# Optimization experiments

Measured on AMD Instinct MI355X. Metric: run time of the kernel, lower is better.

The kernel has to match this reference:

```python
import jax, jax.numpy as jnp
import numpy as np

N, E, DIN, D, FE, L, B, M = 10000, 40000, 11, 64, 4, 4, 512, 3


def setup_inputs() -> dict:
    key = jax.random.key(0)
    ks = iter(jax.random.split(key, 24))
    s = lambda *sh: jax.random.normal(next(ks), sh, jnp.float32)
    return {
        "x": s(N, DIN),
        "edge_index": jax.random.randint(next(ks), (2, E), 0, N),
        "edge_attr": jax.random.uniform(next(ks), (E, FE), jnp.float32),
        "batch": jnp.sort(jax.random.randint(next(ks), (N,), 0, B)),
        "W0": s(DIN, D) * 0.1, "b0": jnp.zeros((D,), jnp.float32),
        "Wn1": s(FE, 2 * D) * 0.1, "bn1": jnp.zeros((2 * D,), jnp.float32),
        "Wn2": s(2 * D, D * D) * 0.02, "bn2": jnp.zeros((D * D,), jnp.float32),
        "root": s(L, D, D) * 0.1, "conv_bias": jnp.zeros((L, D), jnp.float32),
        "lstm_Wih": s(4 * D, 2 * D) * 0.1, "lstm_Whh": s(4 * D, D) * 0.1,
        "lstm_b": jnp.zeros((4 * D,), jnp.float32),
        "Wo1": s(2 * D, D) * 0.1, "bo1": jnp.zeros((D,), jnp.float32),
        "Wo2": s(D, 1) * 0.1, "bo2": jnp.zeros((1,), jnp.float32),
    }


def reference(x, edge_index, edge_attr, batch, W0, b0, Wn1, bn1, Wn2, bn2,
              root, conv_bias, lstm_Wih, lstm_Whh, lstm_b, Wo1, bo1, Wo2, bo2):
    src, dst = edge_index[0], edge_index[1]
    h = x @ W0 + b0  # [N, D]
    # Edge MLP is SHARED across all conv layers -> compute per-edge weight matrices once
    ew = (jax.nn.silu(edge_attr @ Wn1 + bn1) @ Wn2 + bn2).reshape(E, D, D)
    for l in range(L):
        msg = jnp.einsum('ed,edf->ef', h[src], ew)  # gather-compute per edge
        aggr = jax.ops.segment_sum(msg, dst, num_segments=N)  # scatter-add to targets
        h = h + (aggr + h @ root[l] + conv_bias[l])  # NNConv + residual
    # Set2Set pooling (LSTM, M processing steps)
    q_star = jnp.zeros((B, 2 * D), h.dtype)
    hs = jnp.zeros((B, D), h.dtype)
    cs = jnp.zeros((B, D), h.dtype)
    for _ in range(M):
        gates = q_star @ lstm_Wih.T + hs @ lstm_Whh.T + lstm_b
        i, f, g, o = jnp.split(gates, 4, axis=-1)  # torch LSTM gate order
        cs = jax.nn.sigmoid(f) * cs + jax.nn.sigmoid(i) * jnp.tanh(g)
        hs = jax.nn.sigmoid(o) * jnp.tanh(cs)
        q = hs  # [B, D]
        e = jnp.sum(h * q[batch], axis=-1)  # [N]
        emax = jax.ops.segment_max(e, batch, num_segments=B)
        ex = jnp.exp(e - emax[batch])
        denom = jax.ops.segment_sum(ex, batch, num_segments=B)
        a = ex / denom[batch]  # per-graph softmax attention
        r = jax.ops.segment_sum(a[:, None] * h, batch, num_segments=B)
        q_star = jnp.concatenate([q, r], axis=-1)
    out = jax.nn.silu(q_star @ Wo1 + bo1) @ Wo2 + bo2
    return out.reshape(-1)
```

## Files before the change

### kernel.cpp

```cpp
#include <hip/hip_runtime.h>
#include <cstdint>
#include <cstddef>

#define NN   10000
#define EE   40000
#define DIN_ 11
#define DD   64
#define LL   4
#define BB   512
#define MM   3
#define K1   128
#define DD2  4096
#define NPB  16
#define CSPL 2
#define CPB  4
#define ESLOT 12
#define ECREG (8 * ESLOT)
#define EHW (ECREG * 8)

typedef unsigned short ushort_t;
typedef unsigned int   uint_t;

typedef __bf16 bf16x8_t __attribute__((ext_vector_type(8)));
typedef float  f32x4_t  __attribute__((ext_vector_type(4)));
union FragU { uint4 u; bf16x8_t b; };

__device__ __forceinline__ float bfu(ushort_t u) { return __uint_as_float(((uint_t)u) << 16); }
__device__ __forceinline__ float bflo(uint_t u) { return __uint_as_float(u << 16); }
__device__ __forceinline__ float bfhi(uint_t u) { return __uint_as_float(u & 0xffff0000u); }
__device__ __forceinline__ ushort_t f2bf(float f) {
  uint_t u = __float_as_uint(f);
  u = (u + 0x7fffu + ((u >> 16) & 1u)) >> 16;
  return (ushort_t)u;
}
__device__ __forceinline__ uint_t pack2(float lo, float hi) {
  return (uint_t)f2bf(lo) | ((uint_t)f2bf(hi) << 16);
}
__device__ __forceinline__ float sigmf_(float x) { return 1.f / (1.f + expf(-x)); }
__device__ __forceinline__ float siluf_(float x) { return x / (1.f + expf(-x)); }

#if defined(__HIP_DEVICE_COMPILE__) && __has_builtin(__builtin_amdgcn_fdot2_f32_bf16)
typedef __bf16 bf16x2_t __attribute__((ext_vector_type(2)));
__device__ __forceinline__ float dot2a(uint_t a, uint_t b, float c) {
  union { uint_t u; bf16x2_t v; } ua, ub;
  ua.u = a; ub.u = b;
  return __builtin_amdgcn_fdot2_f32_bf16(ua.v, ub.v, c, false);
}
#else
__device__ __forceinline__ float dot2a(uint_t a, uint_t b, float c) {
  return c + bflo(a) * bflo(b) + bfhi(a) * bfhi(b);
}
#endif

#define NCANON 16
struct CanonArgs {
  const void* src[NCANON];
  float* dst[NCANON];
  int n[NCANON];
};
__global__ void k_canon(CanonArgs a, const ushort_t* __restrict__ ea, int* __restrict__ flag) {
  __shared__ int bad;
  if (threadIdx.x == 0) bad = 0;
  __syncthreads();
  ushort_t u = ea[threadIdx.x];
  if ((u & 0x8000u) || u > 0x3F80u) atomicAdd(&bad, 1);
  __syncthreads();
  const int isbf = (bad == 0) ? 1 : 0;
  if (blockIdx.x == 0 && blockIdx.y == 0 && threadIdx.x == 0) *flag = isbf;
  const int ai = blockIdx.y;
  const int n = a.n[ai];
  const int i = blockIdx.x * 256 + threadIdx.x;
  if (i >= n) return;
  float v;
  if (isbf) v = bfu(((const ushort_t*)a.src[ai])[i]);
  else      v = ((const float*)a.src[ai])[i];
  a.dst[ai][i] = v;
}

__global__ void k_wn2m(const void* __restrict__ Wn2, uint_t* __restrict__ out,
                       const int* __restrict__ flag) {
  __shared__ ushort_t row[DD2];
  const int k = blockIdx.x, tid = threadIdx.x;
  if (*flag) {
    const uint4* src = (const uint4*)((const ushort_t*)Wn2 + (size_t)k * DD2);
    ((uint4*)row)[tid] = src[tid];
    ((uint4*)row)[tid + 256] = src[tid + 256];
  } else {
    const float* src = (const float*)Wn2 + (size_t)k * DD2;
    for (int j = 0; j < 16; ++j) row[tid + 256 * j] = f2bf(src[tid + 256 * j]);
  }
  __syncthreads();
  const int kpg = k >> 1, par = k & 1;
  const int lane = tid >> 2, jp = tid & 3;
  const int q = lane >> 4, n = lane & 15;
  for (int fc = 0; fc < 4; ++fc) {
#pragma unroll
    for (int hf = 0; hf < 2; ++hf) {
      int d0 = hf * 32 + q * 8 + 2 * jp;
      int f = fc * 16 + n;
      uint_t lo = row[d0 * 64 + f], hi = row[(d0 + 1) * 64 + f];
      out[((((size_t)kpg * 4 + fc) * 2 + par) * 2 + hf) * 256 + tid] = lo | (hi << 16);
    }
  }
}

__global__ void k_wT(const float* __restrict__ Wihc, const float* __restrict__ Whhc,
                     float* __restrict__ Wiht, float* __restrict__ Whht) {
  int idx = blockIdx.x * 256 + threadIdx.x;
  if (idx < 4 * DD * K1) {
    int j = idx >> 7, i = idx & 127;
    Wiht[i * 256 + j] = Wihc[idx];
  }
  if (idx < 4 * DD * DD) {
    int j = idx >> 6, i = idx & 63;
    Whht[i * 256 + j] = Whhc[idx];
  }
}

__global__ __launch_bounds__(256) void k_embed(
    const float* __restrict__ x, const float* __restrict__ W0,
    const float* __restrict__ b0, const float* __restrict__ bn2,
    float* __restrict__ h, uint_t* __restrict__ hpk,
    float* __restrict__ nbias) {
  __shared__ float xs[4][DIN_];
  __shared__ float hl[4][DD];
  const int tid = threadIdx.x, w = tid >> 6, f = tid & 63;
  const int n = blockIdx.x * 4 + w;
  if (f < DIN_) xs[w][f] = x[n * DIN_ + f];
  __syncthreads();
  float a = b0[f];
  for (int i = 0; i < DIN_; ++i) a += xs[w][i] * W0[i * DD + f];
  h[(size_t)n * DD + f] = a;
  hl[w][f] = a;
  float other = __shfl_down(a, 1);
  if ((f & 1) == 0)
    hpk[(size_t)n * 32 + (f >> 1)] = pack2(a, other);
  __syncthreads();
  float nb = 0.f;
#pragma unroll
  for (int d = 0; d < DD; ++d) nb += hl[w][d] * bn2[d * DD + f];
  nbias[(size_t)n * DD + f] = nb;
}

__global__ void k_edgemlp(const float* __restrict__ ea, const float* __restrict__ Wn1,
                          const float* __restrict__ bn1, const int* __restrict__ epos,
                          uint_t* __restrict__ hn1c) {
  int idx = blockIdx.x * 256 + threadIdx.x;
  if (idx >= EE * (K1 / 2)) return;
  int e = idx >> 6, j = idx & 63;
  int k0 = 2 * j, k1 = 2 * j + 1;
  float a0 = ea[e * 4 + 0], a1 = ea[e * 4 + 1], a2 = ea[e * 4 + 2], a3 = ea[e * 4 + 3];
  float t0 = bn1[k0] + a0 * Wn1[k0] + a1 * Wn1[K1 + k0] + a2 * Wn1[2 * K1 + k0] + a3 * Wn1[3 * K1 + k0];
  float t1 = bn1[k1] + a0 * Wn1[k1] + a1 * Wn1[K1 + k1] + a2 * Wn1[2 * K1 + k1] + a3 * Wn1[3 * K1 + k1];
  int pos = epos[e];
  hn1c[((size_t)(j >> 3) * EE + pos) * 8 + (j & 7)] = pack2(siluf_(t0), siluf_(t1));
}

__global__ void k_hist(const int* __restrict__ ei, int* __restrict__ cnt_s) {
  int e = blockIdx.x * 256 + threadIdx.x;
  if (e >= EE) return;
  atomicAdd(&cnt_s[ei[e]], 1);
}

__global__ void k_scan(const int* __restrict__ cnt, int* __restrict__ rp,
                       const int* __restrict__ batch, int* __restrict__ goff) {
  if (blockIdx.x == 1) {
    int g = threadIdx.x;
    if (g > BB) return;
    int lo = 0, hi = NN;
    while (lo < hi) {
      int mid = (lo + hi) >> 1;
      if (batch[mid] < g) lo = mid + 1; else hi = mid;
    }
    goff[g] = lo;
    return;
  }
  __shared__ int part[1024];
  const int tid = threadIdx.x;
  const int chunk = (NN + 1023) / 1024;
  int s = 0;
  for (int j = 0; j < chunk; ++j) {
    int idx = tid * chunk + j;
    if (idx < NN) s += cnt[idx];
  }
  part[tid] = s;
  __syncthreads();
  for (int off = 1; off < 1024; off <<= 1) {
    int v = (tid >= off) ? part[tid - off] : 0;
    __syncthreads();
    part[tid] += v;
    __syncthreads();
  }
  int base = (tid == 0) ? 0 : part[tid - 1];
  for (int j = 0; j < chunk; ++j) {
    int idx = tid * chunk + j;
    if (idx < NN) { rp[idx] = base; base += cnt[idx]; }
  }
  if (tid == 1023) rp[NN] = part[1023];
}

__global__ void k_fill(const int* __restrict__ ei, const int* __restrict__ rps,
                       int* __restrict__ cur_s, int* __restrict__ epos,
                       int* __restrict__ esd) {
  int e = blockIdx.x * 256 + threadIdx.x;
  if (e >= EE) return;
  int s = ei[e], d = ei[EE + e];
  int ps = atomicAdd(&cur_s[s], 1);
  int pos = rps[s] + ps;
  epos[e] = pos;
  esd[2 * pos] = s;
  esd[2 * pos + 1] = d;
}

__global__ __launch_bounds__(512, 4) void k_conv(
    const uint_t* __restrict__ hpk, const uint_t* __restrict__ hn1c,
    const uint_t* __restrict__ Wn2m, const float* __restrict__ nbias,
    const int* __restrict__ rps, const int* __restrict__ esd,
    float* __restrict__ aggr) {
  __shared__ __align__(16) uint_t Gp[NPB * 2 * 64 * 4];
  __shared__ __align__(16) uint_t eh[CPB * EHW];
  __shared__ int2 eStage[ECREG];
  const int tid = threadIdx.x;
  const int w = tid >> 6, lane = tid & 63;
  const int q = lane >> 4, n16 = lane & 15;
  const int half = blockIdx.x / 625;
  const int ng = blockIdx.x - half * 625;
  const int n0 = ng * NPB;
  const int e0 = rps[n0], e1 = rps[n0 + NPB];
  const int ecnt = e1 - e0;
  const int ecap = ecnt < ECREG ? ecnt : ECREG;

  if (tid < ECREG && tid < ecnt) eStage[tid] = ((const int2*)esd)[e0 + tid];

  uint4 st0, st1, st2, st3;
  const bool stv = (tid < ecap * 2);
  if (stv) {
    const size_t base = ((size_t)(half * CPB) * EE + e0) * 8;
    st0 = ((const uint4*)(hn1c + base))[tid];
    st1 = ((const uint4*)(hn1c + base + (size_t)EE * 8))[tid];
    st2 = ((const uint4*)(hn1c + base + (size_t)2 * EE * 8))[tid];
    st3 = ((const uint4*)(hn1c + base + (size_t)3 * EE * 8))[tid];
  }

  FragU a0, a1;
  {
    const uint4* ap = (const uint4*)(hpk + (size_t)(n0 + n16) * 32);
    a0.u = ap[q];
    a1.u = ap[4 + q];
  }
  __syncthreads();

  float acc[ESLOT];
#pragma unroll
  for (int s = 0; s < ESLOT; ++s) {
    const int li = w + 8 * s;
    float v = 0.f;
    if (half == 0 && li < ecap)
      v = nbias[(size_t)eStage[li].x * 64 + lane];
    acc[s] = v;
  }

  if (stv) {
    ((uint4*)(eh + 0 * EHW))[tid] = st0;
    ((uint4*)(eh + 1 * EHW))[tid] = st1;
    ((uint4*)(eh + 2 * EHW))[tid] = st2;
    ((uint4*)(eh + 3 * EHW))[tid] = st3;
  }

  const int kq = w >> 2, fcw = w & 3;
  for (int cc = 0; cc < CPB; ++cc) {
    const int c = half * CPB + cc;
    if (cc) __syncthreads();
    uint_t pk[4][4];
#pragma unroll
    for (int slot = 0; slot < 4; ++slot) {
      const int kpg = c * 8 + kq * 4 + slot;
      const uint4* bp = (const uint4*)Wn2m + (size_t)(kpg * 4 + fcw) * 256 + lane;
      FragU b00, b01, b10, b11;
      b00.u = bp[0];
      b01.u = bp[64];
      b10.u = bp[128];
      b11.u = bp[192];
      f32x4_t acc0 = {0.f, 0.f, 0.f, 0.f};
      f32x4_t acc1 = {0.f, 0.f, 0.f, 0.f};
      acc0 = __builtin_amdgcn_mfma_f32_16x16x32_bf16(a0.b, b00.b, acc0, 0, 0, 0);
      acc0 = __builtin_amdgcn_mfma_f32_16x16x32_bf16(a1.b, b01.b, acc0, 0, 0, 0);
      acc1 = __builtin_amdgcn_mfma_f32_16x16x32_bf16(a0.b, b10.b, acc1, 0, 0, 0);
      acc1 = __builtin_amdgcn_mfma_f32_16x16x32_bf16(a1.b, b11.b, acc1, 0, 0, 0);
#pragma unroll
      for (int r = 0; r < 4; ++r) pk[r][slot] = pack2(acc0[r], acc1[r]);
    }
#pragma unroll
    for (int r = 0; r < 4; ++r) {
      const int m = q * 4 + r;
      uint4 v;
      v.x = pk[r][0]; v.y = pk[r][1]; v.z = pk[r][2]; v.w = pk[r][3];
      ((uint4*)Gp)[(size_t)(m * 2 + kq) * 64 + fcw * 16 + n16] = v;
    }
    __syncthreads();
    const uint4* ehb = (const uint4*)(eh + cc * EHW);
#pragma unroll
    for (int s = 0; s < ESLOT; ++s) {
      const int li = w + 8 * s;
      if (li < ecap) {
        const int2 sd = eStage[li];
        const int m = sd.x - n0;
        uint4 hv0 = ehb[li * 2], hv1 = ehb[li * 2 + 1];
        const uint4* gb = (const uint4*)Gp + (size_t)(m * 2) * 64 + lane;
        uint4 g0 = gb[0], g1 = gb[64];
        float p = acc[s];
        p = dot2a(g0.x, hv0.x, p);
        p = dot2a(g0.y, hv0.y, p);
        p = dot2a(g0.z, hv0.z, p);
        p = dot2a(g0.w, hv0.w, p);
        p = dot2a(g1.x, hv1.x, p);
        p = dot2a(g1.y, hv1.y, p);
        p = dot2a(g1.z, hv1.z, p);
        p = dot2a(g1.w, hv1.w, p);
        acc[s] = p;
      }
    }
    for (int li = ECREG + w; li < ecnt; li += 8) {
      const int ii = e0 + li;
      const int src = __builtin_amdgcn_readfirstlane(esd[2 * ii]);
      const int dst = __builtin_amdgcn_readfirstlane(esd[2 * ii + 1]);
      const int m = src - n0;
      float p = (half == 0 && cc == 0) ? nbias[(size_t)src * 64 + lane] : 0.f;
      const uint4* hp = (const uint4*)(hn1c + ((size_t)c * EE + ii) * 8);
      uint4 hv0 = hp[0], hv1 = hp[1];
      const uint4* gb = (const uint4*)Gp + (size_t)(m * 2) * 64 + lane;
      uint4 g0 = gb[0], g1 = gb[64];
      p = dot2a(g0.x, hv0.x, p);
      p = dot2a(g0.y, hv0.y, p);
      p = dot2a(g0.z, hv0.z, p);
      p = dot2a(g0.w, hv0.w, p);
      p = dot2a(g1.x, hv1.x, p);
      p = dot2a(g1.y, hv1.y, p);
      p = dot2a(g1.z, hv1.z, p);
      p = dot2a(g1.w, hv1.w, p);
      atomicAdd(&aggr[(size_t)dst * 64 + lane], p);
    }
  }
#pragma unroll
  for (int s = 0; s < ESLOT; ++s) {
    const int li = w + 8 * s;
    if (li < ecap) {
      const int dst = eStage[li].y;
      atomicAdd(&aggr[(size_t)dst * 64 + lane], acc[s]);
    }
  }
}

__global__ __launch_bounds__(256) void k_update(
    float* __restrict__ h, uint_t* __restrict__ hpk,
    float* __restrict__ aggr, const float* __restrict__ bn2,
    const float* __restrict__ root, const float* __restrict__ cb,
    float* __restrict__ nbias, int l) {
  __shared__ float hl[4][DD];
  __shared__ float al[4][DD];
  const int tid = threadIdx.x, w = tid >> 6, f = tid & 63;
  const int n = blockIdx.x * 4 + w;
  float hv = h[(size_t)n * DD + f];
  hl[w][f] = hv;
  float acc = hv + aggr[(size_t)n * DD + f] + cb[l * DD + f];
  aggr[(size_t)n * DD + f] = 0.f;
  __syncthreads();
  const float* rp = root + (size_t)l * DD2;
#pragma unroll
  for (int d = 0; d < DD; ++d) acc += hl[w][d] * rp[d * DD + f];
  h[(size_t)n * DD + f] = acc;
  al[w][f] = acc;
  float other = __shfl_down(acc, 1);
  if ((f & 1) == 0)
    hpk[(size_t)n * 32 + (f >> 1)] = pack2(acc, other);
  __syncthreads();
  float nb = 0.f;
#pragma unroll
  for (int d = 0; d < DD; ++d) nb += al[w][d] * bn2[d * DD + f];
  nbias[(size_t)n * DD + f] = nb;
}

#define EVCAP 2048
__global__ void k_s2s(const float* __restrict__ h, const int* __restrict__ goff,
                      const float* __restrict__ Wiht, const float* __restrict__ Whht,
                      const float* __restrict__ lb,
                      const float* __restrict__ Wo1, const float* __restrict__ bo1,
                      const float* __restrict__ Wo2, const float* __restrict__ bo2,
                      void* __restrict__ outv, const int* __restrict__ flag) {
  __shared__ float qsl[K1];
  __shared__ float hsl[DD];
  __shared__ float csl[DD];
  __shared__ float gl[4][DD];
  __shared__ float ev[EVCAP];
  __shared__ float rp4[4][DD];
  __shared__ float smax, ssum;
  const int g = blockIdx.x, tid = threadIdx.x;
  const int w = tid >> 6, lane = tid & 63;

  if (tid < K1) qsl[tid] = 0.f;
  else if (tid < K1 + DD) hsl[tid - K1] = 0.f;
  else csl[tid - K1 - DD] = 0.f;
  __syncthreads();

  const int i0 = goff[g];
  int cnt = goff[g + 1] - i0;
  if (cnt > EVCAP) cnt = EVCAP;

  for (int m = 0; m < MM; ++m) {
    {
      float a = lb[tid];
      for (int i = 0; i < K1; ++i) a += qsl[i] * Wiht[i * 256 + tid];
      for (int i = 0; i < DD; ++i) a += hsl[i] * Whht[i * 256 + tid];
      gl[tid >> 6][tid & 63] = a;
    }
    __syncthreads();
    if (tid < DD) {
      float ig = sigmf_(gl[0][tid]), fg = sigmf_(gl[1][tid]);
      float gg = tanhf(gl[2][tid]), og = sigmf_(gl[3][tid]);
      float c = fg * csl[tid] + ig * gg;
      csl[tid] = c;
      hsl[tid] = og * tanhf(c);
    }
    __syncthreads();
    const float qv = hsl[lane];
    for (int base = 0; base < cnt; base += 4) {
      const int j = base + w;
      float e = 0.f;
      if (j < cnt) e = h[(size_t)(i0 + j) * DD + lane] * qv;
#pragma unroll
      for (int off = 32; off > 0; off >>= 1) e += __shfl_down(e, off);
      if (lane == 0 && j < cnt) ev[j] = e;
    }
    __syncthreads();
    if (w == 0) {
      float lm = -1e30f;
      for (int jj = lane; jj < cnt; jj += 64) lm = fmaxf(lm, ev[jj]);
#pragma unroll
      for (int off = 32; off > 0; off >>= 1) lm = fmaxf(lm, __shfl_down(lm, off));
      const float emax = __shfl(lm, 0);
      float ls = 0.f;
      for (int jj = lane; jj < cnt; jj += 64) {
        float ex = expf(ev[jj] - emax);
        ev[jj] = ex;
        ls += ex;
      }
#pragma unroll
      for (int off = 32; off > 0; off >>= 1) ls += __shfl_down(ls, off);
      if (lane == 0) { smax = emax; ssum = ls; }
    }
    __syncthreads();
    const float denom = ssum;
    float racc = 0.f;
    for (int jj = w; jj < cnt; jj += 4)
      racc += ev[jj] * h[(size_t)(i0 + jj) * DD + lane];
    rp4[w][lane] = racc;
    __syncthreads();
    if (tid < DD) {
      float r = rp4[0][tid] + rp4[1][tid] + rp4[2][tid] + rp4[3][tid];
      r = (cnt > 0 && denom > 0.f) ? r / denom : 0.f;
      qsl[tid] = hsl[tid];
      qsl[DD + tid] = r;
    }
    __syncthreads();
  }
  if (tid < DD) {
    float t = bo1[tid];
    for (int i = 0; i < K1; ++i) t += qsl[i] * Wo1[i * DD + tid];
    float s = siluf_(t) * Wo2[tid];
    for (int off = 32; off > 0; off >>= 1) s += __shfl_down(s, off);
    if (tid == 0) {
      float v = s + bo2[0];
      if (*flag) ((ushort_t*)outv)[g] = f2bf(v);
      else       ((float*)outv)[g] = v;
    }
  }
}

extern "C" void kernel_launch(void* const* d_in, const int* in_sizes, int n_in,
                              void* d_out, int out_size, void* d_ws, size_t ws_size,
                              hipStream_t stream) {
  const void* x_r    = d_in[0];
  const int*  ei     = (const int*)d_in[1];
  const void* ea_r   = d_in[2];
  const int*  batch  = (const int*)d_in[3];
  const void* W0_r   = d_in[4];
  const void* b0_r   = d_in[5];
  const void* Wn1_r  = d_in[6];
  const void* bn1_r  = d_in[7];
  const void* Wn2_r  = d_in[8];
  const void* bn2_r  = d_in[9];
  const void* root_r = d_in[10];
  const void* cb_r   = d_in[11];
  const void* Wih_r  = d_in[12];
  const void* Whh_r  = d_in[13];
  const void* lb_r   = d_in[14];
  const void* Wo1_r  = d_in[15];
  const void* bo1_r  = d_in[16];
  const void* Wo2_r  = d_in[17];
  const void* bo2_r  = d_in[18];

  char* w = (char*)d_ws;
  size_t off = 0;
  auto alloc = [&](size_t bytes) -> void* {
    void* p = w + off;
    off = (off + bytes + 255) & ~(size_t)255;
    return p;
  };
  int* flag = (int*)alloc(4);
  float* xc    = (float*)alloc((size_t)NN * DIN_ * 4);
  float* eac   = (float*)alloc((size_t)EE * 4 * 4);
  float* W0c   = (float*)alloc((size_t)DIN_ * DD * 4);
  float* b0c   = (float*)alloc((size_t)DD * 4);
  float* Wn1c  = (float*)alloc((size_t)4 * K1 * 4);
  float* bn1c  = (float*)alloc((size_t)K1 * 4);
  float* bn2c  = (float*)alloc((size_t)DD2 * 4);
  float* rootc = (float*)alloc((size_t)LL * DD2 * 4);
  float* cbc   = (float*)alloc((size_t)LL * DD * 4);
  float* Wihc  = (float*)alloc((size_t)4 * DD * K1 * 4);
  float* Whhc  = (float*)alloc((size_t)4 * DD * DD * 4);
  float* lbc   = (float*)alloc((size_t)4 * DD * 4);
  float* Wo1c  = (float*)alloc((size_t)K1 * DD * 4);
  float* bo1c  = (float*)alloc((size_t)DD * 4);
  float* Wo2c  = (float*)alloc((size_t)DD * 4);
  float* bo2c  = (float*)alloc((size_t)4);
  float* Wiht  = (float*)alloc((size_t)K1 * 256 * 4);
  float* Whht  = (float*)alloc((size_t)DD * 256 * 4);
  uint_t* Wn2m = (uint_t*)alloc((size_t)64 * 4 * 2 * 2 * 64 * 4 * 4);
  float*  h    = (float*)alloc((size_t)NN * DD * 4);
  uint_t* hpk  = (uint_t*)alloc((size_t)NN * 32 * 4);
  uint_t* hn1c = (uint_t*)alloc((size_t)EE * (K1 / 2) * 4);
  float*  aggr = (float*)alloc((size_t)NN * DD * 4);
  float*  nbias= (float*)alloc((size_t)NN * DD * 4);
  int* cnts  = (int*)alloc((size_t)2 * NN * 4);
  int* rps   = (int*)alloc((size_t)(NN + 1) * 4);
  int* epos  = (int*)alloc((size_t)EE * 4);
  int* esd   = (int*)alloc((size_t)2 * EE * 4);
  int* goff  = (int*)alloc((size_t)(BB + 1) * 4);

  int* cnt_s = cnts;
  int* cur_s = cnts + NN;

  hipMemsetAsync(cnts, 0, (size_t)2 * NN * 4, stream);
  hipMemsetAsync(aggr, 0, (size_t)NN * DD * 4, stream);

  CanonArgs ca;
  const void* srcs[NCANON] = {x_r, ea_r, W0_r, b0_r, Wn1_r, bn1_r, bn2_r, root_r,
                              cb_r, Wih_r, Whh_r, lb_r, Wo1_r, bo1_r, Wo2_r, bo2_r};
  float* dsts[NCANON] = {xc, eac, W0c, b0c, Wn1c, bn1c, bn2c, rootc,
                         cbc, Wihc, Whhc, lbc, Wo1c, bo1c, Wo2c, bo2c};
  int cnts_c[NCANON] = {NN * DIN_, EE * 4, DIN_ * DD, DD, 4 * K1, K1, DD2, LL * DD2,
                        LL * DD, 4 * DD * K1, 4 * DD * DD, 4 * DD, K1 * DD, DD, DD, 1};
  for (int i = 0; i < NCANON; ++i) { ca.src[i] = srcs[i]; ca.dst[i] = dsts[i]; ca.n[i] = cnts_c[i]; }
  {
    dim3 grid((EE * 4 + 255) / 256, NCANON);
    k_canon<<<grid, 256, 0, stream>>>(ca, (const ushort_t*)ea_r, flag);
  }
  k_wn2m<<<K1, 256, 0, stream>>>(Wn2_r, Wn2m, flag);
  k_wT<<<(4 * DD * K1 + 255) / 256, 256, 0, stream>>>(Wihc, Whhc, Wiht, Whht);

  k_embed<<<NN / 4, 256, 0, stream>>>(xc, W0c, b0c, bn2c, h, hpk, nbias);
  k_hist<<<(EE + 255) / 256, 256, 0, stream>>>(ei, cnt_s);
  k_scan<<<2, 1024, 0, stream>>>(cnt_s, rps, batch, goff);
  k_fill<<<(EE + 255) / 256, 256, 0, stream>>>(ei, rps, cur_s, epos, esd);
  k_edgemlp<<<(EE * (K1 / 2) + 255) / 256, 256, 0, stream>>>(eac, Wn1c, bn1c, epos, hn1c);

  for (int l = 0; l < LL; ++l) {
    k_conv<<<CSPL * (NN / NPB), 512, 0, stream>>>(hpk, hn1c, Wn2m, nbias, rps, esd, aggr);
    k_update<<<NN / 4, 256, 0, stream>>>(h, hpk, aggr, bn2c, rootc, cbc, nbias, l);
  }

  k_s2s<<<BB, 256, 0, stream>>>(h, goff, Wiht, Whht, lbc, Wo1c, bo1c, Wo2c, bo2c,
                                d_out, flag);
}
```

Measured before the change: 409.5 us.

## Bucket edges into fixed per-source-node slots so conv warps reuse node G

k_fill now also writes a padded per-node slot table with up to DEGCAP outgoing edges per source node (destination and CSR position), initialised to -1. In k_conv each warp owns two fixed source nodes, so it loads their G rows from LDS once and reuses them across all slot edges. This replaces the per-edge G gathers and the variable-length edge staging. Empty slots do wasted dot products, and edges past the cap go through a fallback loop that scans every edge of the block. That loop reloads esd and rps per edge and per chunk, which adds global traffic for high-degree nodes.

```diff
diff --git a/kernel.cpp b/kernel.cpp
--- a/kernel.cpp
+++ b/kernel.cpp
@@ -14,9 +14,9 @@
 #define NPB  16
 #define CSPL 2
 #define CPB  4
+#define DEGCAP 6
+#define NSLOT (NPB * DEGCAP)
 #define ESLOT 12
-#define ECREG (8 * ESLOT)
-#define EHW (ECREG * 8)
 
 typedef unsigned short ushort_t;
 typedef unsigned int   uint_t;
@@ -201,7 +201,7 @@
 
 __global__ void k_fill(const int* __restrict__ ei, const int* __restrict__ rps,
                        int* __restrict__ cur_s, int* __restrict__ epos,
-                       int* __restrict__ esd) {
+                       int* __restrict__ esd, int2* __restrict__ slot2) {
   int e = blockIdx.x * 256 + threadIdx.x;
   if (e >= EE) return;
   int s = ei[e], d = ei[EE + e];
@@ -210,37 +210,38 @@
   epos[e] = pos;
   esd[2 * pos] = s;
   esd[2 * pos + 1] = d;
+  if (ps < DEGCAP)
+    slot2[(size_t)(s >> 4) * NSLOT + (s & 15) * DEGCAP + ps] = make_int2(d, pos);
 }
 
 __global__ __launch_bounds__(512, 4) void k_conv(
     const uint_t* __restrict__ hpk, const uint_t* __restrict__ hn1c,
     const uint_t* __restrict__ Wn2m, const float* __restrict__ nbias,
     const int* __restrict__ rps, const int* __restrict__ esd,
-    float* __restrict__ aggr) {
+    const int2* __restrict__ slot2, float* __restrict__ aggr) {
   __shared__ __align__(16) uint_t Gp[NPB * 2 * 64 * 4];
-  __shared__ __align__(16) uint_t eh[CPB * EHW];
-  __shared__ int2 eStage[ECREG];
+  __shared__ __align__(16) uint_t eh[CPB * NSLOT * 8];
+  __shared__ int eDst[NSLOT];
   const int tid = threadIdx.x;
   const int w = tid >> 6, lane = tid & 63;
   const int q = lane >> 4, n16 = lane & 15;
   const int half = blockIdx.x / 625;
   const int ng = blockIdx.x - half * 625;
   const int n0 = ng * NPB;
-  const int e0 = rps[n0], e1 = rps[n0 + NPB];
-  const int ecnt = e1 - e0;
-  const int ecap = ecnt < ECREG ? ecnt : ECREG;
-
-  if (tid < ECREG && tid < ecnt) eStage[tid] = ((const int2*)esd)[e0 + tid];
-
-  uint4 st0, st1, st2, st3;
-  const bool stv = (tid < ecap * 2);
-  if (stv) {
-    const size_t base = ((size_t)(half * CPB) * EE + e0) * 8;
-    st0 = ((const uint4*)(hn1c + base))[tid];
-    st1 = ((const uint4*)(hn1c + base + (size_t)EE * 8))[tid];
-    st2 = ((const uint4*)(hn1c + base + (size_t)2 * EE * 8))[tid];
-    st3 = ((const uint4*)(hn1c + base + (size_t)3 * EE * 8))[tid];
-  }
+  const int2* sl = slot2 + (size_t)ng * NSLOT;
+
+  uint4 st0 = {}, st1 = {}, st2 = {}, st3 = {};
+  if (tid < 2 * NSLOT) {
+    const int spos = sl[tid >> 1].y;
+    if (spos >= 0) {
+      const size_t b = ((size_t)(half * CPB) * EE + spos) * 8 + (size_t)(tid & 1) * 4;
+      st0 = *(const uint4*)(hn1c + b);
+      st1 = *(const uint4*)(hn1c + b + (size_t)EE * 8);
+      st2 = *(const uint4*)(hn1c + b + (size_t)2 * EE * 8);
+      st3 = *(const uint4*)(hn1c + b + (size_t)3 * EE * 8);
+    }
+  }
+  if (tid < NSLOT) eDst[tid] = sl[tid].x;
 
   FragU a0, a1;
   {
@@ -248,24 +249,29 @@
     a0.u = ap[q];
     a1.u = ap[4 + q];
   }
-  __syncthreads();
+
+  float nb0 = 0.f, nb1 = 0.f;
+  if (half == 0) {
+    nb0 = nbias[(size_t)(n0 + 2 * w) * 64 + lane];
+    nb1 = nbias[(size_t)(n0 + 2 * w + 1) * 64 + lane];
+  }
+
+  if (tid < 2 * NSLOT) {
+    uint_t* ep = eh + (tid >> 1) * 8 + (tid & 1) * 4;
+    *(uint4*)(ep) = st0;
+    *(uint4*)(ep + NSLOT * 8) = st1;
+    *(uint4*)(ep + 2 * NSLOT * 8) = st2;
+    *(uint4*)(ep + 3 * NSLOT * 8) = st3;
+  }
 
   float acc[ESLOT];
 #pragma unroll
-  for (int s = 0; s < ESLOT; ++s) {
-    const int li = w + 8 * s;
-    float v = 0.f;
-    if (half == 0 && li < ecap)
-      v = nbias[(size_t)eStage[li].x * 64 + lane];
-    acc[s] = v;
-  }
-
-  if (stv) {
-    ((uint4*)(eh + 0 * EHW))[tid] = st0;
-    ((uint4*)(eh + 1 * EHW))[tid] = st1;
-    ((uint4*)(eh + 2 * EHW))[tid] = st2;
-    ((uint4*)(eh + 3 * EHW))[tid] = st3;
-  }
+  for (int s = 0; s < DEGCAP; ++s) acc[s] = nb0;
+#pragma unroll
+  for (int s = DEGCAP; s < ESLOT; ++s) acc[s] = nb1;
+
+  const int e0 = rps[n0], e1 = rps[n0 + NPB];
+  const int ecnt = e1 - e0;
 
   const int kq = w >> 2, fcw = w & 3;
   for (int cc = 0; cc < CPB; ++cc) {
@@ -298,35 +304,50 @@
       ((uint4*)Gp)[(size_t)(m * 2 + kq) * 64 + fcw * 16 + n16] = v;
     }
     __syncthreads();
-    const uint4* ehb = (const uint4*)(eh + cc * EHW);
-#pragma unroll
-    for (int s = 0; s < ESLOT; ++s) {
-      const int li = w + 8 * s;
-      if (li < ecap) {
-        const int2 sd = eStage[li];
-        const int m = sd.x - n0;
-        uint4 hv0 = ehb[li * 2], hv1 = ehb[li * 2 + 1];
-        const uint4* gb = (const uint4*)Gp + (size_t)(m * 2) * 64 + lane;
-        uint4 g0 = gb[0], g1 = gb[64];
+    const uint4* ehb = (const uint4*)(eh + cc * NSLOT * 8);
+    {
+      const uint4* gA = (const uint4*)Gp + (size_t)(4 * w) * 64 + lane;
+      const uint4* gB = (const uint4*)Gp + (size_t)(4 * w + 2) * 64 + lane;
+      uint4 gA0 = gA[0], gA1 = gA[64];
+      uint4 gB0 = gB[0], gB1 = gB[64];
+#pragma unroll
+      for (int s = 0; s < DEGCAP; ++s) {
+        uint4 hv0 = ehb[(ESLOT * w + s) * 2], hv1 = ehb[(ESLOT * w + s) * 2 + 1];
         float p = acc[s];
-        p = dot2a(g0.x, hv0.x, p);
-        p = dot2a(g0.y, hv0.y, p);
-        p = dot2a(g0.z, hv0.z, p);
-        p = dot2a(g0.w, hv0.w, p);
-        p = dot2a(g1.x, hv1.x, p);
-        p = dot2a(g1.y, hv1.y, p);
-        p = dot2a(g1.z, hv1.z, p);
-        p = dot2a(g1.w, hv1.w, p);
+        p = dot2a(gA0.x, hv0.x, p);
+        p = dot2a(gA0.y, hv0.y, p);
+        p = dot2a(gA0.z, hv0.z, p);
+        p = dot2a(gA0.w, hv0.w, p);
+        p = dot2a(gA1.x, hv1.x, p);
+        p = dot2a(gA1.y, hv1.y, p);
+        p = dot2a(gA1.z, hv1.z, p);
+        p = dot2a(gA1.w, hv1.w, p);
         acc[s] = p;
       }
-    }
-    for (int li = ECREG + w; li < ecnt; li += 8) {
-      const int ii = e0 + li;
-      const int src = __builtin_amdgcn_readfirstlane(esd[2 * ii]);
-      const int dst = __builtin_amdgcn_readfirstlane(esd[2 * ii + 1]);
+#pragma unroll
+      for (int s = 0; s < DEGCAP; ++s) {
+        uint4 hv0 = ehb[(ESLOT * w + DEGCAP + s) * 2];
+        uint4 hv1 = ehb[(ESLOT * w + DEGCAP + s) * 2 + 1];
+        float p = acc[DEGCAP + s];
+        p = dot2a(gB0.x, hv0.x, p);
+        p = dot2a(gB0.y, hv0.y, p);
+        p = dot2a(gB0.z, hv0.z, p);
+        p = dot2a(gB0.w, hv0.w, p);
+        p = dot2a(gB1.x, hv1.x, p);
+        p = dot2a(gB1.y, hv1.y, p);
+        p = dot2a(gB1.z, hv1.z, p);
+        p = dot2a(gB1.w, hv1.w, p);
+        acc[DEGCAP + s] = p;
+      }
+    }
+    for (int li = w; li < ecnt; li += 8) {
+      const int pos = e0 + li;
+      const int src = __builtin_amdgcn_readfirstlane(esd[2 * pos]);
+      if (pos - rps[src] < DEGCAP) continue;
+      const int dst = __builtin_amdgcn_readfirstlane(esd[2 * pos + 1]);
       const int m = src - n0;
       float p = (half == 0 && cc == 0) ? nbias[(size_t)src * 64 + lane] : 0.f;
-      const uint4* hp = (const uint4*)(hn1c + ((size_t)c * EE + ii) * 8);
+      const uint4* hp = (const uint4*)(hn1c + ((size_t)c * EE + pos) * 8);
       uint4 hv0 = hp[0], hv1 = hp[1];
       const uint4* gb = (const uint4*)Gp + (size_t)(m * 2) * 64 + lane;
       uint4 g0 = gb[0], g1 = gb[64];
@@ -343,11 +364,8 @@
   }
 #pragma unroll
   for (int s = 0; s < ESLOT; ++s) {
-    const int li = w + 8 * s;
-    if (li < ecap) {
-      const int dst = eStage[li].y;
-      atomicAdd(&aggr[(size_t)dst * 64 + lane], acc[s]);
-    }
+    const int dst = eDst[ESLOT * w + s];
+    if (dst >= 0) atomicAdd(&aggr[(size_t)dst * 64 + lane], acc[s]);
   }
 }
 
@@ -536,12 +554,14 @@
   int* epos  = (int*)alloc((size_t)EE * 4);
   int* esd   = (int*)alloc((size_t)2 * EE * 4);
   int* goff  = (int*)alloc((size_t)(BB + 1) * 4);
+  int2* slot2 = (int2*)alloc((size_t)(NN / NPB) * NSLOT * 8);
 
   int* cnt_s = cnts;
   int* cur_s = cnts + NN;
 
   hipMemsetAsync(cnts, 0, (size_t)2 * NN * 4, stream);
   hipMemsetAsync(aggr, 0, (size_t)NN * DD * 4, stream);
+  hipMemsetAsync(slot2, 0xFF, (size_t)(NN / NPB) * NSLOT * 8, stream);
 
   CanonArgs ca;
   const void* srcs[NCANON] = {x_r, ea_r, W0_r, b0_r, Wn1_r, bn1_r, bn2_r, root_r,
@@ -561,11 +581,11 @@
   k_embed<<<NN / 4, 256, 0, stream>>>(xc, W0c, b0c, bn2c, h, hpk, nbias);
   k_hist<<<(EE + 255) / 256, 256, 0, stream>>>(ei, cnt_s);
   k_scan<<<2, 1024, 0, stream>>>(cnt_s, rps, batch, goff);
-  k_fill<<<(EE + 255) / 256, 256, 0, stream>>>(ei, rps, cur_s, epos, esd);
+  k_fill<<<(EE + 255) / 256, 256, 0, stream>>>(ei, rps, cur_s, epos, esd, slot2);
   k_edgemlp<<<(EE * (K1 / 2) + 255) / 256, 256, 0, stream>>>(eac, Wn1c, bn1c, epos, hn1c);
 
   for (int l = 0; l < LL; ++l) {
-    k_conv<<<CSPL * (NN / NPB), 512, 0, stream>>>(hpk, hn1c, Wn2m, nbias, rps, esd, aggr);
+    k_conv<<<CSPL * (NN / NPB), 512, 0, stream>>>(hpk, hn1c, Wn2m, nbias, rps, esd, slot2, aggr);
     k_update<<<NN / 4, 256, 0, stream>>>(h, hpk, aggr, bn2c, rootc, cbc, nbias, l);
   }
 
```

Result: slower. 1.080 ms (+163.9%).
